# Optimization experiments

Hardware: AMD Instinct MI355X
Metric: run time of the kernel (lower is better)

Reference implementation:

```python
import jax, jax.numpy as jnp
import numpy as np

LN_EPS = 1e-3  # keras LayerNormalization default epsilon
LEAKY_SLOPE = 0.2  # tf 'leaky_relu' default alpha


def layer_norm(x, gamma, beta):
    mu = jnp.mean(x, axis=-1, keepdims=True)
    var = jnp.mean(jnp.square(x - mu), axis=-1, keepdims=True)
    return (x - mu) * jax.lax.rsqrt(var + LN_EPS) * gamma + beta


def attention_head(q_in, kv_in, Wk, Wv, Wq, causal):
    # q_in: [b, sq, d], kv_in: [b, sk, d]
    K = jnp.einsum('bsd,de->bse', kv_in, Wk)
    V = jnp.einsum('bsd,de->bse', kv_in, Wv)
    Q = jnp.einsum('bsd,de->bse', q_in, Wq)
    sk = K.shape[1]
    # NOTE: original scales by sqrt(window_size_keys), i.e. key seq length
    scores = jnp.einsum('bqe,bke->bqk', Q, K) / jnp.sqrt(jnp.float32(sk))
    if causal:
        sq = Q.shape[1]
        mask = jnp.triu(jnp.full((sq, sk), -jnp.inf, dtype=scores.dtype), k=1)
        scores = scores + mask
    probs = jax.nn.softmax(scores, axis=-1)
    return jnp.einsum('bqk,bke->bqe', probs, V)


def setup_inputs() -> dict:
    key = jax.random.key(0)
    ks = jax.random.split(key, 12)
    B, S, D, H = 4, 4096, 256, 400
    p = lambda k, shp: jax.random.normal(k, shp, dtype=jnp.float32) * 0.1
    return {
        'inputs': jax.random.normal(ks[0], (B, S, D), dtype=jnp.float32),
        'context_sequence': jax.random.normal(ks[1], (B, S, D), dtype=jnp.float32),
        'sa_Wk': p(ks[2], (D, D)),
        'sa_Wv': p(ks[3], (D, D)),
        'sa_Wq': p(ks[4], (D, D)),
        'ca_Wk': p(ks[5], (D, D)),
        'ca_Wv': p(ks[6], (D, D)),
        'ca_Wq': p(ks[7], (D, D)),
        'W1': p(ks[8], (D, H)),
        'b1': jnp.zeros((H,), dtype=jnp.float32),
        'W2': p(ks[9], (H, D)),
        'b2': jnp.zeros((D,), dtype=jnp.float32),
        'gamma': jnp.ones((D,), dtype=jnp.float32),
        'beta': jnp.zeros((D,), dtype=jnp.float32),
    }


def reference(inputs, context_sequence, sa_Wk, sa_Wv, sa_Wq, ca_Wk, ca_Wv, ca_Wq,
              W1, b1, W2, b2, gamma, beta):
    # 1) masked self-attention + residual + LN (shared LN params)
    in_attn = attention_head(inputs, inputs, sa_Wk, sa_Wv, sa_Wq, causal=True)
    x = layer_norm(in_attn + inputs, gamma, beta)
    # 2) unmasked cross-attention (queries = x, keys/values = context) + residual + LN
    ctx_attn = attention_head(x, context_sequence, ca_Wk, ca_Wv, ca_Wq, causal=False)
    y = layer_norm(ctx_attn + x, gamma, beta)
    # 3) FFN (Dense 400 leaky_relu -> Dense emb) + residual + LN
    h = jax.nn.leaky_relu(jnp.einsum('bsd,dh->bsh', y, W1) + b1, negative_slope=LEAKY_SLOPE)
    ff = jnp.einsum('bsh,hd->bsd', h, W2) + b2
    return layer_norm(ff + y, gamma, beta)
```

## Files before the change

### kernel.cpp

```cpp
#include <hip/hip_runtime.h>

typedef __bf16  bf16x4 __attribute__((ext_vector_type(4)));
typedef __bf16  bf16x8 __attribute__((ext_vector_type(8)));
typedef float   f32x4  __attribute__((ext_vector_type(4)));
typedef unsigned int u32;

constexpr int BM = 128, BN = 128, BK = 32;

__device__ __forceinline__ void async_cp16(const __bf16* g, __bf16* lds) {
    __builtin_amdgcn_global_load_lds(
        (const __attribute__((address_space(1))) u32*)g,
        (__attribute__((address_space(3))) u32*)lds, 16, 0, 0);
}

__device__ __forceinline__ int swz(int row, int q) {
    return row * BK + (((q + (row >> 1)) & 3) << 3);
}

#define ASM_LGKM0 asm volatile("s_waitcnt lgkmcnt(0)" ::: "memory")
#define ASM_VM8   asm volatile("s_waitcnt vmcnt(8)" ::: "memory")
#define ASM_VM0   asm volatile("s_waitcnt vmcnt(0)" ::: "memory")
#define SBAR()    do { __builtin_amdgcn_s_barrier(); asm volatile("" ::: "memory"); } while (0)

template<int EPI>
__launch_bounds__(256)
__global__ void gemm_nt(const __bf16* __restrict__ Aall, const __bf16* __restrict__ Ball,
                        const float* __restrict__ bias,
                        void* __restrict__ C0, void* __restrict__ C1, void* __restrict__ C2,
                        int N, int K, long ldb, long sA, long sB, long sC,
                        int nTx, int klen, long pstrideB)
{
    const int bx = blockIdx.x;
    const int chunk = bx / nTx;
    const int n0 = (bx - chunk * nTx) * BN;
    const int m0 = blockIdx.y * BM;
    const int bz = blockIdx.z;
    const int kbase = chunk * klen;

    const __bf16* A  = Aall + (long)bz * sA;
    const __bf16* Bt = Ball + (long)bz * sB;

    __shared__ alignas(16) __bf16 As[BM * BK];
    __shared__ alignas(16) __bf16 Bs[BN * BK];

    const int tid = threadIdx.x;
    const int wave = tid >> 6, lane = tid & 63;
    const int wm = (wave >> 1) * 64, wn = (wave & 1) * 64;
    const int quad = lane >> 4, l16 = lane & 15;

    const int row0 = tid >> 2, sl0 = tid & 3;
    const int ks0 = (sl0 - (row0 >> 1)) & 3;
    const int row1 = row0 + 64;
    const int ks1 = (sl0 - (row1 >> 1)) & 3;
    const __bf16* gA0 = A  + (long)(m0 + row0) * K + kbase + ks0 * 8;
    const __bf16* gA1 = A  + (long)(m0 + row1) * K + kbase + ks1 * 8;
    const __bf16* gB0 = Bt + (long)(n0 + row0) * ldb + kbase + ks0 * 8;
    const __bf16* gB1 = Bt + (long)(n0 + row1) * ldb + kbase + ks1 * 8;
    __bf16* ldsA0 = As + wave * 512;
    __bf16* ldsA1 = As + 2048 + wave * 512;
    __bf16* ldsB0 = Bs + wave * 512;
    __bf16* ldsB1 = Bs + 2048 + wave * 512;

    f32x4 acc[4][4];
    #pragma unroll
    for (int i = 0; i < 4; i++)
        #pragma unroll
        for (int j = 0; j < 4; j++) { f32x4 z = {0.f, 0.f, 0.f, 0.f}; acc[i][j] = z; }

    for (int kk = 0; kk < klen; kk += BK) {
        __syncthreads();
        async_cp16(gA0, ldsA0);
        async_cp16(gA1, ldsA1);
        async_cp16(gB0, ldsB0);
        async_cp16(gB1, ldsB1);
        gA0 += BK; gA1 += BK; gB0 += BK; gB1 += BK;
        __syncthreads();

        bf16x8 af[4], bg[4];
        #pragma unroll
        for (int i = 0; i < 4; i++) {
            af[i] = *(const bf16x8*)(As + swz(wm + i * 16 + l16, quad));
            bg[i] = *(const bf16x8*)(Bs + swz(wn + i * 16 + l16, quad));
        }
        #pragma unroll
        for (int i = 0; i < 4; i++)
            #pragma unroll
            for (int j = 0; j < 4; j++)
                acc[i][j] = __builtin_amdgcn_mfma_f32_16x16x32_bf16(af[i], bg[j], acc[i][j], 0, 0, 0);
    }

    char* cb = (char*)C0 + (EPI == 3 ? (long)chunk * pstrideB : 0);
    #pragma unroll
    for (int j = 0; j < 4; j++) {
        const int col = n0 + wn + j * 16 + l16;
        const float bv = (EPI == 2) ? bias[col] : 0.f;
        #pragma unroll
        for (int i = 0; i < 4; i++) {
            #pragma unroll
            for (int r = 0; r < 4; r++) {
                const int row = m0 + wm + i * 16 + quad * 4 + r;
                float c = acc[i][j][r];
                if (EPI == 2) { c += bv; c = c > 0.f ? c : 0.2f * c; }
                if (EPI == 1 || EPI == 3)
                    ((__bf16*)cb)[(long)bz * sC + (long)row * N + col] = (__bf16)c;
                else if (EPI == 2)
                    ((__bf16*)cb)[(long)row * N + col] = (__bf16)c;
                else {
                    const int seg = col >> 8;
                    __bf16* dst = seg == 0 ? (__bf16*)C0 : (seg == 1 ? (__bf16*)C1 : (__bf16*)C2);
                    dst[(long)row * 256 + (col & 255)] = (__bf16)c;
                }
            }
        }
    }
}

template<int CAUSAL>
__launch_bounds__(512, 2)
__global__ void fattn(const __bf16* __restrict__ Qall, const __bf16* __restrict__ Kall,
                      const __bf16* __restrict__ Vt,
                      __bf16* __restrict__ pbuf, float* __restrict__ side,
                      int NS, long pstrideE, float scale)
{
    constexpr int S = 4096, D = 256, R = 16384;
    const int mt = CAUSAL ? (int)(gridDim.x - 1 - blockIdx.x) : (int)blockIdx.x;
    const int chunk = blockIdx.y;
    const int bz = blockIdx.z;
    const int m0 = mt * 128;

    const int T = CAUSAL ? ((m0 + 128) >> 6) : (S >> 6);
    const int t0 = chunk * T / NS;
    const int t1 = (chunk + 1) * T / NS;
    const int kbase = t0 << 6;
    const int ntile = t1 - t0;

    const __bf16* Q  = Qall + ((long)bz * S + m0) * D;
    const __bf16* Kp = Kall + (long)bz * S * D;
    const long vcol0 = (long)bz * S;

    __shared__ alignas(16) __bf16 Ks[2][16384];
    __shared__ alignas(16) __bf16 Vs[2][16384];
    __shared__ alignas(16) __bf16 Ps[128 * 64];
    __shared__ float sred[8][32];

    const int tid = threadIdx.x;
    const int wave = tid >> 6, lane = tid & 63;
    const int quad = lane >> 4, l16 = lane & 15;
    const int wq32 = (wave >> 1) * 32;
    const int wk = (wave & 1) * 32;
    const int we = (wave & 1) * 128;

    bf16x8 qf[2][8];
    #pragma unroll
    for (int i = 0; i < 2; i++)
        #pragma unroll
        for (int kd = 0; kd < 8; kd++)
            qf[i][kd] = *(const bf16x8*)(Q + (long)(wq32 + i * 16 + l16) * D + kd * 32 + quad * 8);

    const int srowK = (tid >> 2) & 63;
    const int srowV = tid >> 2;
    const int ks8 = (((tid & 3) - (tid >> 3)) & 3) << 3;
    const int wbase = (tid & ~63) * 8;

    f32x4 acc[2][8];
    #pragma unroll
    for (int i = 0; i < 2; i++)
        #pragma unroll
        for (int j = 0; j < 8; j++) { f32x4 z = {0.f, 0.f, 0.f, 0.f}; acc[i][j] = z; }
    float se[2][4] = {{0.f,0.f,0.f,0.f},{0.f,0.f,0.f,0.f}};

    auto stage = [&](int buf, int kb) {
        const __bf16* gK = Kp + (long)(kb + srowK) * D + ks8 + ((tid >> 8) << 5);
        #pragma unroll
        for (int c = 0; c < 4; c++)
            async_cp16(gK + c * 64, Ks[buf] + c * 4096 + wbase);
        const __bf16* gV = Vt + vcol0 + kb + ks8;
        #pragma unroll
        for (int c = 0; c < 4; c++)
            async_cp16(gV + (long)(((c & 1) << 7) + srowV) * R + ((c >> 1) << 5),
                       Vs[buf] + c * 4096 + wbase);
    };

    if (ntile > 0) {
        stage(0, kbase);
        if (ntile > 1) { stage(1, kbase + 64); ASM_VM8; }
        else           { ASM_VM0; }
        SBAR();
    }

    for (int t = 0; t < ntile; ++t) {
        const int cur = t & 1;
        const int kb = kbase + (t << 6);
        const __bf16* Kb_ = Ks[cur];
        const __bf16* Vb_ = Vs[cur];

        f32x4 sacc[2][2];
        #pragma unroll
        for (int i = 0; i < 2; i++)
            #pragma unroll
            for (int j = 0; j < 2; j++) { f32x4 z = {0.f, 0.f, 0.f, 0.f}; sacc[i][j] = z; }
        __builtin_amdgcn_s_setprio(1);
        #pragma unroll
        for (int kd = 0; kd < 8; kd++) {
            bf16x8 b0 = *(const bf16x8*)(Kb_ + kd * 2048 + swz(wk + l16, quad));
            bf16x8 b1 = *(const bf16x8*)(Kb_ + kd * 2048 + swz(wk + 16 + l16, quad));
            sacc[0][0] = __builtin_amdgcn_mfma_f32_16x16x32_bf16(qf[0][kd], b0, sacc[0][0], 0, 0, 0);
            sacc[1][0] = __builtin_amdgcn_mfma_f32_16x16x32_bf16(qf[1][kd], b0, sacc[1][0], 0, 0, 0);
            sacc[0][1] = __builtin_amdgcn_mfma_f32_16x16x32_bf16(qf[0][kd], b1, sacc[0][1], 0, 0, 0);
            sacc[1][1] = __builtin_amdgcn_mfma_f32_16x16x32_bf16(qf[1][kd], b1, sacc[1][1], 0, 0, 0);
        }
        __builtin_amdgcn_s_setprio(0);

        const bool diag = CAUSAL && (kb >= m0);
        #pragma unroll
        for (int i = 0; i < 2; i++)
            #pragma unroll
            for (int j = 0; j < 2; j++) {
                const int kloc = wk + j * 16 + l16;
                #pragma unroll
                for (int r = 0; r < 4; r++) {
                    const int qloc = wq32 + i * 16 + quad * 4 + r;
                    float e = __expf(sacc[i][j][r] * scale);
                    if (diag && kb + kloc > m0 + qloc) e = 0.f;
                    se[i][r] += e;
                    Ps[qloc * 64 + (((kloc >> 3) ^ (qloc & 7)) << 3) + (kloc & 7)] = (__bf16)e;
                }
            }
        ASM_LGKM0; SBAR();

        __builtin_amdgcn_s_setprio(1);
        #pragma unroll
        for (int kc = 0; kc < 2; kc++) {
            const int sx = (kc * 4 + quad) ^ (l16 & 7);
            bf16x8 pa0 = *(const bf16x8*)(Ps + (wq32 + l16) * 64 + (sx << 3));
            bf16x8 pa1 = *(const bf16x8*)(Ps + (wq32 + 16 + l16) * 64 + (sx << 3));
            #pragma unroll
            for (int jn = 0; jn < 8; jn++) {
                bf16x8 vb = *(const bf16x8*)(Vb_ + kc * 8192 + swz(we + jn * 16 + l16, quad));
                acc[0][jn] = __builtin_amdgcn_mfma_f32_16x16x32_bf16(pa0, vb, acc[0][jn], 0, 0, 0);
                acc[1][jn] = __builtin_amdgcn_mfma_f32_16x16x32_bf16(pa1, vb, acc[1][jn], 0, 0, 0);
            }
        }
        __builtin_amdgcn_s_setprio(0);
        ASM_LGKM0; SBAR();

        if (t + 1 < ntile) {
            if (t + 2 < ntile) { stage(cur, kbase + ((t + 2) << 6)); ASM_VM8; }
            else               { ASM_VM0; }
            SBAR();
        }
    }

    #pragma unroll
    for (int st = 1; st < 16; st <<= 1)
        #pragma unroll
        for (int i = 0; i < 2; i++)
            #pragma unroll
            for (int r = 0; r < 4; r++) se[i][r] += __shfl_xor(se[i][r], st);
    if (l16 == 0)
        #pragma unroll
        for (int i = 0; i < 2; i++)
            #pragma unroll
            for (int r = 0; r < 4; r++)
                sred[wave][i * 16 + quad * 4 + r] = se[i][r];
    __syncthreads();
    if ((wave & 1) == 0 && l16 == 0) {
        float* sd = side + ((long)bz * 64 + chunk) * 4096 + m0 + wq32;
        #pragma unroll
        for (int i = 0; i < 2; i++)
            #pragma unroll
            for (int r = 0; r < 4; r++) {
                const int idx = i * 16 + quad * 4 + r;
                sd[idx] = sred[wave][idx] + sred[wave + 1][idx];
            }
    }

    __bf16* cb = pbuf + (long)chunk * pstrideE + ((long)bz * S + m0) * D;
    #pragma unroll
    for (int jn = 0; jn < 8; jn++) {
        const int col = we + jn * 16 + l16;
        #pragma unroll
        for (int i = 0; i < 2; i++)
            #pragma unroll
            for (int r = 0; r < 4; r++)
                cb[(long)(wq32 + i * 16 + quad * 4 + r) * D + col] = (__bf16)acc[i][jn][r];
    }
}

__global__ void reduce_inv_n(const float* __restrict__ side, float* __restrict__ inv, int lim)
{
    const int i = blockIdx.x * 256 + threadIdx.x;
    const int b = i >> 12, r = i & 4095;
    const float* sp = side + (long)b * 64 * 4096 + r;
    float s = 0.f;
    for (int t = 0; t < lim; t++) s += sp[(long)t * 4096];
    inv[i] = 1.f / s;
}

template<int NP>
__launch_bounds__(256)
__global__ void ln_res(const __bf16* __restrict__ p, long pstr,
                       const float* __restrict__ resid, const float* __restrict__ invs,
                       const float* __restrict__ bias,
                       const float* __restrict__ gamma, const float* __restrict__ beta,
                       float* __restrict__ outf, __bf16* __restrict__ outb)
{
    const int row  = blockIdx.x * 4 + (threadIdx.x >> 6);
    const int lane = threadIdx.x & 63;
    const long vi = (long)row * 64 + lane;
    float p0 = 0.f, p1 = 0.f, p2 = 0.f, p3 = 0.f;
    #pragma unroll
    for (int i = 0; i < NP; i++) {
        bf16x4 vp = ((const bf16x4*)(p + (long)i * pstr))[vi];
        p0 += (float)vp[0]; p1 += (float)vp[1]; p2 += (float)vp[2]; p3 += (float)vp[3];
    }
    if (invs) { const float iv = invs[row]; p0 *= iv; p1 *= iv; p2 *= iv; p3 *= iv; }
    float4 vr = ((const float4*)resid)[vi];
    float x0 = vr.x + p0, x1 = vr.y + p1, x2 = vr.z + p2, x3 = vr.w + p3;
    if (bias) {
        float4 vb = ((const float4*)bias)[lane];
        x0 += vb.x; x1 += vb.y; x2 += vb.z; x3 += vb.w;
    }
    float s = x0 + x1 + x2 + x3;
    #pragma unroll
    for (int off = 32; off; off >>= 1) s += __shfl_xor(s, off);
    const float mu = s * (1.f / 256.f);
    float d0 = x0 - mu, d1 = x1 - mu, d2 = x2 - mu, d3 = x3 - mu;
    float s2 = d0 * d0 + d1 * d1 + d2 * d2 + d3 * d3;
    #pragma unroll
    for (int off = 32; off; off >>= 1) s2 += __shfl_xor(s2, off);
    const float rs = rsqrtf(s2 * (1.f / 256.f) + 1e-3f);
    const float4 g  = ((const float4*)gamma)[lane];
    const float4 be = ((const float4*)beta)[lane];
    float o0 = d0 * rs * g.x + be.x, o1 = d1 * rs * g.y + be.y;
    float o2 = d2 * rs * g.z + be.z, o3 = d3 * rs * g.w + be.w;
    float4 o; o.x = o0; o.y = o1; o.z = o2; o.w = o3;
    ((float4*)outf)[vi] = o;
    if (outb) {
        bf16x4 ob; ob[0] = (__bf16)o0; ob[1] = (__bf16)o1; ob[2] = (__bf16)o2; ob[3] = (__bf16)o3;
        ((bf16x4*)outb)[vi] = ob;
    }
}

__device__ __forceinline__ void tp(const float* __restrict__ src, __bf16* __restrict__ dst,
                                   int rows, int cols, int rowsP, int i)
{
    const int c = i / rowsP, r = i - c * rowsP;
    const float v = (r < rows && c < cols) ? src[r * cols + c] : 0.f;
    dst[i] = (__bf16)v;
}

__global__ void prep_all(const float4* __restrict__ inA, const float4* __restrict__ inC,
                         bf16x4* __restrict__ outA, bf16x4* __restrict__ outC,
                         const float* __restrict__ sWq, const float* __restrict__ sWk,
                         const float* __restrict__ sWv,
                         const float* __restrict__ cWq, const float* __restrict__ cWk,
                         const float* __restrict__ cWv,
                         const float* __restrict__ W1, const float* __restrict__ W2,
                         __bf16* __restrict__ wqk_s, __bf16* __restrict__ wv_s,
                         __bf16* __restrict__ wq_c, __bf16* __restrict__ wk_c,
                         __bf16* __restrict__ wv_c,
                         __bf16* __restrict__ W1t, __bf16* __restrict__ W2t,
                         const float* __restrict__ b1, float* __restrict__ b1p)
{
    const int bx = blockIdx.x, tid = threadIdx.x;
    if (bx < 8192) {
        const bool a = bx < 4096;
        const long j = (long)(a ? bx : bx - 4096) * 256 + tid;
        float4 v = (a ? inA : inC)[j];
        bf16x4 o; o[0] = (__bf16)v.x; o[1] = (__bf16)v.y; o[2] = (__bf16)v.z; o[3] = (__bf16)v.w;
        (a ? outA : outC)[j] = o;
    }
    else if (bx < 8448)  tp(sWq, wqk_s,          256, 256, 256, (bx - 8192)  * 256 + tid);
    else if (bx < 8704)  tp(sWk, wqk_s + 65536,  256, 256, 256, (bx - 8448)  * 256 + tid);
    else if (bx < 8960)  tp(sWv, wv_s,           256, 256, 256, (bx - 8704)  * 256 + tid);
    else if (bx < 9216)  tp(cWq, wq_c,           256, 256, 256, (bx - 8960)  * 256 + tid);
    else if (bx < 9472)  tp(cWk, wk_c,           256, 256, 256, (bx - 9216)  * 256 + tid);
    else if (bx < 9728)  tp(cWv, wv_c,           256, 256, 256, (bx - 9472)  * 256 + tid);
    else if (bx < 10240) tp(W1,  W1t,            256, 400, 256, (bx - 9728)  * 256 + tid);
    else if (bx < 10752) tp(W2,  W2t,            400, 256, 512, (bx - 10240) * 256 + tid);
    else { const int i = (bx - 10752) * 256 + tid; if (i < 512) b1p[i] = (i < 400) ? b1[i] : 0.f; }
}

extern "C" void kernel_launch(void* const* d_in, const int* in_sizes, int n_in,
                              void* d_out, int out_size, void* d_ws, size_t ws_size,
                              hipStream_t stream)
{
    constexpr int B = 4, S = 4096, D = 256, H = 400, Hp = 512;
    constexpr int R = B * S;
    constexpr float SCALE = 1.f / 64.f;
    constexpr int NSc = 4;
    constexpr int NSx = 2;
    constexpr int NSf = 2;

    const float* inputs = (const float*)d_in[0];
    const float* ctx    = (const float*)d_in[1];
    const float* sa_Wk  = (const float*)d_in[2];
    const float* sa_Wv  = (const float*)d_in[3];
    const float* sa_Wq  = (const float*)d_in[4];
    const float* ca_Wk  = (const float*)d_in[5];
    const float* ca_Wv  = (const float*)d_in[6];
    const float* ca_Wq  = (const float*)d_in[7];
    const float* W1     = (const float*)d_in[8];
    const float* b1     = (const float*)d_in[9];
    const float* W2     = (const float*)d_in[10];
    const float* b2     = (const float*)d_in[11];
    const float* gamma  = (const float*)d_in[12];
    const float* beta   = (const float*)d_in[13];
    float* out = (float*)d_out;

    char* ws = (char*)d_ws;
    size_t off = 0;
    auto alloc = [&](size_t bytes) -> char* {
        char* p = ws + off; off += (bytes + 255) & ~size_t(255); return p;
    };
    __bf16* bfA  = (__bf16*)alloc((size_t)R * D * 2);
    __bf16* bfC  = (__bf16*)alloc((size_t)R * D * 2);
    __bf16* Qb   = (__bf16*)alloc((size_t)R * D * 2);
    __bf16* Kb   = (__bf16*)alloc((size_t)R * D * 2);
    __bf16* Vt   = (__bf16*)alloc((size_t)D * R * 2);
    __bf16* h    = (__bf16*)alloc((size_t)R * Hp * 2);
    float*  x    = (float*)alloc((size_t)R * D * 4);
    float*  y    = (float*)alloc((size_t)R * D * 4);
    float*  side = (float*)alloc((size_t)B * 64 * S * 4);
    float*  invb = (float*)alloc((size_t)B * S * 4);
    __bf16* wqk_s = (__bf16*)alloc((size_t)2 * D * D * 2);
    __bf16* wv_s  = (__bf16*)alloc((size_t)D * D * 2);
    __bf16* wq_c  = (__bf16*)alloc((size_t)D * D * 2);
    __bf16* wk_c  = (__bf16*)alloc((size_t)D * D * 2);
    __bf16* wv_c  = (__bf16*)alloc((size_t)D * D * 2);
    __bf16* W1t  = (__bf16*)alloc((size_t)Hp * D * 2);
    __bf16* W2t  = (__bf16*)alloc((size_t)D * Hp * 2);
    float*  b1p  = (float*)alloc((size_t)Hp * 4);

    const size_t PBb = (size_t)R * D * 2;
    __bf16* pbuf = (__bf16*)alloc((size_t)4 * PBb);
    if (off > ws_size) return;
    const long PBe = (long)R * D;

    __bf16* xbf = bfA;
    __bf16* ybf = bfC;

    const dim3 blk(256);
    const dim3 blk512(512);

    auto launch_ln = [&](int np, const float* res, const float* invs, const float* bias,
                         float* of, __bf16* ob) {
        if (np == 4)      ln_res<4><<<R / 4, blk, 0, stream>>>(pbuf, PBe, res, invs, bias, gamma, beta, of, ob);
        else if (np == 2) ln_res<2><<<R / 4, blk, 0, stream>>>(pbuf, PBe, res, invs, bias, gamma, beta, of, ob);
        else              ln_res<1><<<R / 4, blk, 0, stream>>>(pbuf, PBe, res, invs, bias, gamma, beta, of, ob);
    };

    prep_all<<<10754, blk, 0, stream>>>((const float4*)inputs, (const float4*)ctx,
        (bf16x4*)bfA, (bf16x4*)bfC, sa_Wq, sa_Wk, sa_Wv, ca_Wq, ca_Wk, ca_Wv, W1, W2,
        wqk_s, wv_s, wq_c, wk_c, wv_c, W1t, W2t, b1, b1p);

    gemm_nt<4><<<dim3(4, 128, 1), blk, 0, stream>>>(bfA, wqk_s, nullptr,
        Qb, Kb, nullptr, 2 * D, D, D, 0, 0, 0, 4, D, 0);
    gemm_nt<1><<<dim3(128, 2, 1), blk, 0, stream>>>(wv_s, bfA, nullptr,
        Vt, nullptr, nullptr, R, D, D, 0, 0, 0, 128, D, 0);
    fattn<1><<<dim3(32, NSc, B), blk512, 0, stream>>>(Qb, Kb, Vt, pbuf, side, NSc, PBe, SCALE);
    reduce_inv_n<<<R / 256, blk, 0, stream>>>(side, invb, NSc);
    launch_ln(NSc, inputs, invb, nullptr, x, xbf);

    gemm_nt<1><<<dim3(2, 128, 1), blk, 0, stream>>>(xbf, wq_c, nullptr,
        Qb, nullptr, nullptr, D, D, D, 0, 0, 0, 2, D, 0);
    gemm_nt<1><<<dim3(2, 128, 1), blk, 0, stream>>>(bfC, wk_c, nullptr,
        Kb, nullptr, nullptr, D, D, D, 0, 0, 0, 2, D, 0);
    gemm_nt<1><<<dim3(128, 2, 1), blk, 0, stream>>>(wv_c, bfC, nullptr,
        Vt, nullptr, nullptr, R, D, D, 0, 0, 0, 128, D, 0);
    fattn<0><<<dim3(32, NSx, B), blk512, 0, stream>>>(Qb, Kb, Vt, pbuf, side, NSx, PBe, SCALE);
    reduce_inv_n<<<R / 256, blk, 0, stream>>>(side, invb, NSx);
    launch_ln(NSx, x, invb, nullptr, y, ybf);

    gemm_nt<2><<<dim3(4, 128, 1), blk, 0, stream>>>(ybf, W1t, b1p,
        h, nullptr, nullptr, Hp, D, D, 0, 0, 0, 4, D, 0);
    gemm_nt<3><<<dim3(2 * NSf, 128, 1), blk, 0, stream>>>(h, W2t, nullptr,
        pbuf, nullptr, nullptr, D, Hp, Hp, 0, 0, 0, 2, Hp / NSf, (long)PBb);
    launch_ln(NSf, y, nullptr, b2, out, nullptr);
}
```

Baseline: 406.8 us.

## Fuse softmax-denominator reduction into LayerNorm and batch projection GEMMs via z-dimension

Removes the separate reduce_inv_n kernels by summing the per-chunk softmax denominators inside ln_res. Batches the self- and cross-attention V projections into one launch with gridDim.z=2, writing into a doubled Vt buffer. The cross-attention Q and K projections also share one batched launch, which relies on the bfA/bfC and Qb/Kb buffers and the wq_c/wk_c weights being adjacent in memory; wv_c was moved next to wv_s for the same reason. This cuts kernel launches and lets the cross V projection run earlier, at the cost of every wave redundantly loading the side sums (64 lanes per row) and a dependence on workspace layout strides.

```diff
diff --git a/kernel.cpp b/kernel.cpp
--- a/kernel.cpp
+++ b/kernel.cpp
@@ -287,20 +287,11 @@
     }
 }
 
-__global__ void reduce_inv_n(const float* __restrict__ side, float* __restrict__ inv, int lim)
-{
-    const int i = blockIdx.x * 256 + threadIdx.x;
-    const int b = i >> 12, r = i & 4095;
-    const float* sp = side + (long)b * 64 * 4096 + r;
-    float s = 0.f;
-    for (int t = 0; t < lim; t++) s += sp[(long)t * 4096];
-    inv[i] = 1.f / s;
-}
-
 template<int NP>
 __launch_bounds__(256)
 __global__ void ln_res(const __bf16* __restrict__ p, long pstr,
-                       const float* __restrict__ resid, const float* __restrict__ invs,
+                       const float* __restrict__ resid,
+                       const float* __restrict__ side, int lim,
                        const float* __restrict__ bias,
                        const float* __restrict__ gamma, const float* __restrict__ beta,
                        float* __restrict__ outf, __bf16* __restrict__ outb)
@@ -314,7 +305,13 @@
         bf16x4 vp = ((const bf16x4*)(p + (long)i * pstr))[vi];
         p0 += (float)vp[0]; p1 += (float)vp[1]; p2 += (float)vp[2]; p3 += (float)vp[3];
     }
-    if (invs) { const float iv = invs[row]; p0 *= iv; p1 *= iv; p2 *= iv; p3 *= iv; }
+    if (side) {
+        const float* sp = side + (long)(row >> 12) * 64 * 4096 + (row & 4095);
+        float sv = 0.f;
+        for (int t = 0; t < lim; t++) sv += sp[(long)t * 4096];
+        const float iv = 1.f / sv;
+        p0 *= iv; p1 *= iv; p2 *= iv; p3 *= iv;
+    }
     float4 vr = ((const float4*)resid)[vi];
     float x0 = vr.x + p0, x1 = vr.y + p1, x2 = vr.z + p2, x3 = vr.w + p3;
     if (bias) {
@@ -418,17 +415,16 @@
     __bf16* bfC  = (__bf16*)alloc((size_t)R * D * 2);
     __bf16* Qb   = (__bf16*)alloc((size_t)R * D * 2);
     __bf16* Kb   = (__bf16*)alloc((size_t)R * D * 2);
-    __bf16* Vt   = (__bf16*)alloc((size_t)D * R * 2);
+    __bf16* Vt   = (__bf16*)alloc((size_t)2 * D * R * 2);
     __bf16* h    = (__bf16*)alloc((size_t)R * Hp * 2);
     float*  x    = (float*)alloc((size_t)R * D * 4);
     float*  y    = (float*)alloc((size_t)R * D * 4);
     float*  side = (float*)alloc((size_t)B * 64 * S * 4);
-    float*  invb = (float*)alloc((size_t)B * S * 4);
     __bf16* wqk_s = (__bf16*)alloc((size_t)2 * D * D * 2);
     __bf16* wv_s  = (__bf16*)alloc((size_t)D * D * 2);
+    __bf16* wv_c  = (__bf16*)alloc((size_t)D * D * 2);
     __bf16* wq_c  = (__bf16*)alloc((size_t)D * D * 2);
     __bf16* wk_c  = (__bf16*)alloc((size_t)D * D * 2);
-    __bf16* wv_c  = (__bf16*)alloc((size_t)D * D * 2);
     __bf16* W1t  = (__bf16*)alloc((size_t)Hp * D * 2);
     __bf16* W2t  = (__bf16*)alloc((size_t)D * Hp * 2);
     float*  b1p  = (float*)alloc((size_t)Hp * 4);
@@ -444,11 +440,11 @@
     const dim3 blk(256);
     const dim3 blk512(512);
 
-    auto launch_ln = [&](int np, const float* res, const float* invs, const float* bias,
-                         float* of, __bf16* ob) {
-        if (np == 4)      ln_res<4><<<R / 4, blk, 0, stream>>>(pbuf, PBe, res, invs, bias, gamma, beta, of, ob);
-        else if (np == 2) ln_res<2><<<R / 4, blk, 0, stream>>>(pbuf, PBe, res, invs, bias, gamma, beta, of, ob);
-        else              ln_res<1><<<R / 4, blk, 0, stream>>>(pbuf, PBe, res, invs, bias, gamma, beta, of, ob);
+    auto launch_ln = [&](int np, const float* res, const float* sd, int lim,
+                         const float* bias, float* of, __bf16* ob) {
+        if (np == 4)      ln_res<4><<<R / 4, blk, 0, stream>>>(pbuf, PBe, res, sd, lim, bias, gamma, beta, of, ob);
+        else if (np == 2) ln_res<2><<<R / 4, blk, 0, stream>>>(pbuf, PBe, res, sd, lim, bias, gamma, beta, of, ob);
+        else              ln_res<1><<<R / 4, blk, 0, stream>>>(pbuf, PBe, res, sd, lim, bias, gamma, beta, of, ob);
     };
 
     prep_all<<<10754, blk, 0, stream>>>((const float4*)inputs, (const float4*)ctx,
@@ -457,25 +453,22 @@
 
     gemm_nt<4><<<dim3(4, 128, 1), blk, 0, stream>>>(bfA, wqk_s, nullptr,
         Qb, Kb, nullptr, 2 * D, D, D, 0, 0, 0, 4, D, 0);
-    gemm_nt<1><<<dim3(128, 2, 1), blk, 0, stream>>>(wv_s, bfA, nullptr,
-        Vt, nullptr, nullptr, R, D, D, 0, 0, 0, 128, D, 0);
+    gemm_nt<1><<<dim3(128, 2, 2), blk, 0, stream>>>(wv_s, bfA, nullptr,
+        Vt, nullptr, nullptr, R, D, D, (long)D * D, (long)R * D, (long)D * R, 128, D, 0);
+
     fattn<1><<<dim3(32, NSc, B), blk512, 0, stream>>>(Qb, Kb, Vt, pbuf, side, NSc, PBe, SCALE);
-    reduce_inv_n<<<R / 256, blk, 0, stream>>>(side, invb, NSc);
-    launch_ln(NSc, inputs, invb, nullptr, x, xbf);
-
-    gemm_nt<1><<<dim3(2, 128, 1), blk, 0, stream>>>(xbf, wq_c, nullptr,
-        Qb, nullptr, nullptr, D, D, D, 0, 0, 0, 2, D, 0);
-    gemm_nt<1><<<dim3(2, 128, 1), blk, 0, stream>>>(bfC, wk_c, nullptr,
-        Kb, nullptr, nullptr, D, D, D, 0, 0, 0, 2, D, 0);
-    gemm_nt<1><<<dim3(128, 2, 1), blk, 0, stream>>>(wv_c, bfC, nullptr,
-        Vt, nullptr, nullptr, R, D, D, 0, 0, 0, 128, D, 0);
-    fattn<0><<<dim3(32, NSx, B), blk512, 0, stream>>>(Qb, Kb, Vt, pbuf, side, NSx, PBe, SCALE);
-    reduce_inv_n<<<R / 256, blk, 0, stream>>>(side, invb, NSx);
-    launch_ln(NSx, x, invb, nullptr, y, ybf);
+    launch_ln(NSc, inputs, side, NSc, nullptr, x, xbf);
+
+    gemm_nt<1><<<dim3(2, 128, 2), blk, 0, stream>>>(xbf, wq_c, nullptr,
+        Qb, nullptr, nullptr, D, D, D, (long)R * D, (long)D * D, (long)R * D, 2, D, 0);
+
+    fattn<0><<<dim3(32, NSx, B), blk512, 0, stream>>>(Qb, Kb, Vt + (size_t)D * R,
+        pbuf, side, NSx, PBe, SCALE);
+    launch_ln(NSx, x, side, NSx, nullptr, y, ybf);
 
     gemm_nt<2><<<dim3(4, 128, 1), blk, 0, stream>>>(ybf, W1t, b1p,
         h, nullptr, nullptr, Hp, D, D, 0, 0, 0, 4, D, 0);
     gemm_nt<3><<<dim3(2 * NSf, 128, 1), blk, 0, stream>>>(h, W2t, nullptr,
         pbuf, nullptr, nullptr, D, Hp, Hp, 0, 0, 0, 2, Hp / NSf, (long)PBb);
-    launch_ln(NSf, y, nullptr, b2, out, nullptr);
-}
+    launch_ln(NSf, y, nullptr, 0, b2, out, nullptr);
+}
```

After: 391.2 us. 1.04x faster.
